# Optimization experiments

Measured on AMD Instinct MI355X. Metric: run time of the kernel, lower is better.

The kernel has to match this reference:

```python
import jax, jax.numpy as jnp
import numpy as np

B, N, D, H = 2, 2048, 1024, 16
HD = D // H  # head dim = 64
SCALING = (D / H) ** 0.5  # sqrt(64) = 8
EPS = 1e-5


def setup_inputs() -> dict:
    key = jax.random.key(0)
    k1, k2, k3 = jax.random.split(key, 3)
    return {
        "z": jax.random.normal(k1, (B, N, D), dtype=jnp.float32),
        "ln_scale": jnp.ones((D,), dtype=jnp.float32),
        "ln_bias": jnp.zeros((D,), dtype=jnp.float32),
        "w_qkv": jax.random.normal(k2, (D, 3 * D), dtype=jnp.float32) * (D ** -0.5),
        "w_proj": jax.random.normal(k3, (D, D), dtype=jnp.float32) * (D ** -0.5),
        "b_proj": jnp.zeros((D,), dtype=jnp.float32),
    }


def reference(z, ln_scale, ln_bias, w_qkv, w_proj, b_proj):
    b, n, d = z.shape
    # LayerNorm (pre-norm)
    mu = jnp.mean(z, axis=-1, keepdims=True)
    var = jnp.mean(jnp.square(z - mu), axis=-1, keepdims=True)
    zn = (z - mu) / jnp.sqrt(var + EPS) * ln_scale + ln_bias
    # QKV projection: [b, n, 3D]
    qkv = zn @ w_qkv
    # einops 'b n (h d qkv_n) -> qkv_n b h n d': qkv index is innermost
    qkv5 = qkv.reshape(b, n, H, HD, 3)  # [b, n, h, d, 3]
    q = jnp.transpose(qkv5[..., 0], (0, 2, 1, 3))  # [b, h, n, d]
    k = jnp.transpose(qkv5[..., 1], (0, 2, 1, 3))
    v = jnp.transpose(qkv5[..., 2], (0, 2, 1, 3))
    # Attention: scores scaled AFTER the matmul, as in the source
    scores = jnp.einsum('bhqd,bhkd->bhqk', q, k) / SCALING
    att = jax.nn.softmax(scores, axis=-1)
    out = jnp.einsum('bhal,bhlv->bhav', att, v)  # [b, h, n, d]
    out = jnp.transpose(out, (0, 2, 1, 3)).reshape(b, n, d)  # merge heads
    out = out @ w_proj + b_proj  # projection (dropout p=0)
    return z + out
```

## Files before the change

kernel.cpp:

```cpp
#include <hip/hip_runtime.h>
#include <stdint.h>
#include <math.h>

typedef unsigned short u16;
typedef float f32x4 __attribute__((ext_vector_type(4)));
typedef __bf16 bf16x8 __attribute__((ext_vector_type(8)));

__device__ __forceinline__ u16 f2bf(float f) {
    union { float f; uint32_t u; } c; c.f = f;
    return (u16)((c.u + 0x7FFFu + ((c.u >> 16) & 1u)) >> 16);
}

__device__ __forceinline__ void gload_lds16(const void* g, void* l) {
    __builtin_amdgcn_global_load_lds(
        (const __attribute__((address_space(1))) unsigned int*)g,
        (__attribute__((address_space(3))) unsigned int*)l, 16, 0, 0);
}

__global__ __launch_bounds__(256) void ln_kernel(const float* __restrict__ z,
                                                 const float* __restrict__ sc,
                                                 const float* __restrict__ bs,
                                                 u16* __restrict__ zn) {
    const int row = blockIdx.x, tid = threadIdx.x;
    const float4 v = ((const float4*)(z + row * 1024))[tid];
    float s = v.x + v.y + v.z + v.w;
    #pragma unroll
    for (int off = 32; off > 0; off >>= 1) s += __shfl_xor(s, off);
    __shared__ float red[8];
    if ((tid & 63) == 0) red[tid >> 6] = s;
    __syncthreads();
    const float mean = (red[0] + red[1] + red[2] + red[3]) * (1.0f / 1024.0f);
    const float dx = v.x - mean, dy = v.y - mean, dz = v.z - mean, dw = v.w - mean;
    float q = dx * dx + dy * dy + dz * dz + dw * dw;
    #pragma unroll
    for (int off = 32; off > 0; off >>= 1) q += __shfl_xor(q, off);
    if ((tid & 63) == 0) red[4 + (tid >> 6)] = q;
    __syncthreads();
    const float var = (red[4] + red[5] + red[6] + red[7]) * (1.0f / 1024.0f);
    const float rstd = rsqrtf(var + 1e-5f);
    const float4 scv = ((const float4*)sc)[tid];
    const float4 bsv = ((const float4*)bs)[tid];
    const u16 o0 = f2bf(dx * rstd * scv.x + bsv.x);
    const u16 o1 = f2bf(dy * rstd * scv.y + bsv.y);
    const u16 o2 = f2bf(dz * rstd * scv.z + bsv.z);
    const u16 o3 = f2bf(dw * rstd * scv.w + bsv.w);
    uint2 pk;
    pk.x = (uint32_t)o0 | ((uint32_t)o1 << 16);
    pk.y = (uint32_t)o2 | ((uint32_t)o3 << 16);
    *(uint2*)&zn[row * 1024 + tid * 4] = pk;
}

__global__ __launch_bounds__(256) void transpose_cast(const float* __restrict__ in,
                                                      u16* __restrict__ out,
                                                      int K, int N, int permute) {
    __shared__ float t[32][33];
    const int tid = threadIdx.x;
    const int j = tid & 31, i0 = tid >> 5;
    const int kb = blockIdx.y * 32, nb = blockIdx.x * 32;
    #pragma unroll
    for (int p = 0; p < 4; ++p) {
        int r = i0 + p * 8;
        t[r][j] = in[(size_t)(kb + r) * N + nb + j];
    }
    __syncthreads();
    #pragma unroll
    for (int p = 0; p < 4; ++p) {
        int r = i0 + p * 8;
        int c = nb + r;
        int np = c;
        if (permute) {
            int h = c / 192, rem = c - h * 192;
            int d = rem / 3, s = rem - d * 3;
            np = s * 1024 + h * 64 + d;
        }
        out[(size_t)np * K + kb + j] = f2bf(t[j][r]);
    }
}

__global__ __launch_bounds__(256) void gemm_qkv(const u16* __restrict__ A,
                                                const u16* __restrict__ Bt,
                                                u16* __restrict__ qbuf,
                                                u16* __restrict__ kbuf,
                                                u16* __restrict__ vbuf) {
    __shared__ __align__(16) u16 As[128 * 32];
    __shared__ __align__(16) u16 Bs[128 * 32];
    const int tid = threadIdx.x;
    const int wave = tid >> 6, lane = tid & 63;
    const int quad = lane >> 4, l16 = lane & 15;
    const int wm = (wave >> 1) * 64, wn = (wave & 1) * 64;
    const int row0 = blockIdx.x * 128, col0 = blockIdx.y * 128;
    const int gr = lane >> 2, gc = (lane & 3) * 8;
    f32x4 acc[4][4] = {};
    for (int kt = 0; kt < 1024; kt += 32) {
        __syncthreads();
        #pragma unroll
        for (int i = 0; i < 2; ++i) {
            const int rb = wave * 16 + i * 64;
            gload_lds16(&A[(size_t)(row0 + rb + gr) * 1024 + kt + gc], &As[rb * 32]);
            gload_lds16(&Bt[(size_t)(col0 + rb + gr) * 1024 + kt + gc], &Bs[rb * 32]);
        }
        __syncthreads();
        bf16x8 ax[4], bx[4];
        #pragma unroll
        for (int t = 0; t < 4; ++t) {
            ax[t] = *(const bf16x8*)&As[(wm + t * 16 + l16) * 32 + quad * 8];
            bx[t] = *(const bf16x8*)&Bs[(wn + t * 16 + l16) * 32 + quad * 8];
        }
        #pragma unroll
        for (int mt = 0; mt < 4; ++mt)
            #pragma unroll
            for (int nt = 0; nt < 4; ++nt)
                acc[mt][nt] = __builtin_amdgcn_mfma_f32_16x16x32_bf16(ax[mt], bx[nt], acc[mt][nt], 0, 0, 0);
    }
    const int s = col0 >> 10;
    u16* const dst = (s == 0) ? qbuf : ((s == 1) ? kbuf : vbuf);
    const float scl = (s == 0) ? 0.125f * 1.44269504088896f : 1.0f;
    #pragma unroll
    for (int mt = 0; mt < 4; ++mt) {
        #pragma unroll
        for (int nt = 0; nt < 4; ++nt) {
            #pragma unroll
            for (int e = 0; e < 4; ++e) {
                const int row = row0 + wm + mt * 16 + quad * 4 + e;
                const int col = col0 + wn + nt * 16 + l16;
                const int b = row >> 11, n = row & 2047;
                const int h = (col >> 6) & 15, d = col & 63;
                dst[((size_t)(b * 16 + h) * 2048 + n) * 64 + d] = f2bf(acc[mt][nt][e] * scl);
            }
        }
    }
}

__global__ __launch_bounds__(256) void transpose_v(const u16* __restrict__ vbuf,
                                                   u16* __restrict__ vT) {
    __shared__ u16 t[64][72];
    const int tid = threadIdx.x;
    const int bh = blockIdx.y, nb = blockIdx.x * 64;
    const int r = tid >> 3, c = (tid & 7) * 8;
    #pragma unroll
    for (int i = 0; i < 2; ++i)
        *(uint4*)&t[r + i * 32][c] = *(const uint4*)&vbuf[((size_t)bh * 2048 + nb + r + i * 32) * 64 + c];
    __syncthreads();
    #pragma unroll
    for (int i = 0; i < 2; ++i) {
        const int d = r + i * 32;
        u16 tmp[8];
        #pragma unroll
        for (int j = 0; j < 8; ++j) tmp[j] = t[c + j][d];
        *(uint4*)&vT[((size_t)bh * 64 + d) * 2048 + nb + c] = *(uint4*)tmp;
    }
}

__global__ __launch_bounds__(256) void attn_kernel(const u16* __restrict__ qb,
                                                   const u16* __restrict__ kb,
                                                   const u16* __restrict__ vT,
                                                   u16* __restrict__ att_out) {
    __shared__ __align__(16) u16 Ks[128 * 64];
    __shared__ __align__(16) u16 Vs[64 * 128];
    const int tid = threadIdx.x;
    const int wave = tid >> 6, lane = tid & 63;
    const int quad = lane >> 4, l16 = lane & 15;
    const int qt = blockIdx.x, bh = blockIdx.y;
    const int b = bh >> 4, h = bh & 15;

    const u16* qrowA = &qb[(size_t)(bh * 2048 + qt * 128 + wave * 32 + l16) * 64];
    const bf16x8 qA0 = *(const bf16x8*)&qrowA[quad * 8];
    const bf16x8 qA1 = *(const bf16x8*)&qrowA[32 + quad * 8];
    const u16* qrowB = qrowA + 16 * 64;
    const bf16x8 qB0 = *(const bf16x8*)&qrowB[quad * 8];
    const bf16x8 qB1 = *(const bf16x8*)&qrowB[32 + quad * 8];

    const u16* ksrc[4];
    const u16* vsrc[4];
    #pragma unroll
    for (int j = 0; j < 4; ++j) {
        const int p = 8 * wave + 32 * j + (lane >> 3);
        const int kr = (p & 0x60) | ((p & 12) << 1) | ((p & 16) >> 2) | (p & 3);
        const int gk = (lane & 7) ^ (p & 7);
        ksrc[j] = kb + ((size_t)bh * 2048 + kr) * 64 + gk * 8;
        const int d = 4 * wave + 16 * j + (lane >> 4);
        const int gv = (lane & 15) ^ (d & 15);
        vsrc[j] = vT + ((size_t)bh * 64 + d) * 2048 + gv * 8;
    }

    f32x4 oA[4] = {}, oB[4] = {};
    f32x4 lA = {}, lB = {};
    bf16x8 ones;
    #pragma unroll
    for (int i = 0; i < 8; ++i) ones[i] = (__bf16)1.0f;

    for (int kt = 0; kt < 16; ++kt) {
        __syncthreads();
        #pragma unroll
        for (int j = 0; j < 4; ++j) {
            gload_lds16(ksrc[j], &Ks[(8 * wave + 32 * j) * 64]);
            gload_lds16(vsrc[j], &Vs[(4 * wave + 16 * j) * 128]);
            ksrc[j] += 128 * 64;
            vsrc[j] += 128;
        }
        __syncthreads();

        f32x4 sA[8] = {}, sB[8] = {};
        #pragma unroll
        for (int nt = 0; nt < 8; ++nt) {
            const int r = nt * 16 + l16;
            const bf16x8 k0 = *(const bf16x8*)&Ks[r * 64 + (((quad) ^ (r & 7)) << 3)];
            const bf16x8 k1 = *(const bf16x8*)&Ks[r * 64 + (((quad + 4) ^ (r & 7)) << 3)];
            sA[nt] = __builtin_amdgcn_mfma_f32_16x16x32_bf16(k0, qA0, sA[nt], 0, 0, 0);
            sA[nt] = __builtin_amdgcn_mfma_f32_16x16x32_bf16(k1, qA1, sA[nt], 0, 0, 0);
            sB[nt] = __builtin_amdgcn_mfma_f32_16x16x32_bf16(k0, qB0, sB[nt], 0, 0, 0);
            sB[nt] = __builtin_amdgcn_mfma_f32_16x16x32_bf16(k1, qB1, sB[nt], 0, 0, 0);
        }

        bf16x8 apA[4], apB[4];
        #pragma unroll
        for (int nt = 0; nt < 8; ++nt) {
            #pragma unroll
            for (int e = 0; e < 4; ++e) {
                apA[nt >> 1][(nt & 1) * 4 + e] = (__bf16)exp2f(sA[nt][e]);
                apB[nt >> 1][(nt & 1) * 4 + e] = (__bf16)exp2f(sB[nt][e]);
            }
        }

        #pragma unroll
        for (int vt = 0; vt < 4; ++vt) {
            const int dd = vt * 16 + l16;
            #pragma unroll
            for (int c = 0; c < 4; ++c) {
                const bf16x8 vf = *(const bf16x8*)&Vs[dd * 128 + (((c * 4 + quad) ^ l16) << 3)];
                oA[vt] = __builtin_amdgcn_mfma_f32_16x16x32_bf16(apA[c], vf, oA[vt], 0, 0, 0);
                oB[vt] = __builtin_amdgcn_mfma_f32_16x16x32_bf16(apB[c], vf, oB[vt], 0, 0, 0);
            }
        }
        #pragma unroll
        for (int c = 0; c < 4; ++c) {
            lA = __builtin_amdgcn_mfma_f32_16x16x32_bf16(apA[c], ones, lA, 0, 0, 0);
            lB = __builtin_amdgcn_mfma_f32_16x16x32_bf16(apB[c], ones, lB, 0, 0, 0);
        }
    }

    #pragma unroll
    for (int e = 0; e < 4; ++e) {
        const float invA = 1.0f / lA[e];
        const float invB = 1.0f / lB[e];
        const int nA = qt * 128 + wave * 32 + quad * 4 + e;
        #pragma unroll
        for (int vt = 0; vt < 4; ++vt) {
            att_out[(size_t)(b * 2048 + nA) * 1024 + h * 64 + vt * 16 + l16] = f2bf(oA[vt][e] * invA);
            att_out[(size_t)(b * 2048 + nA + 16) * 1024 + h * 64 + vt * 16 + l16] = f2bf(oB[vt][e] * invB);
        }
    }
}

__global__ __launch_bounds__(256) void gemm_proj(const u16* __restrict__ A,
                                                 const u16* __restrict__ Bt,
                                                 const float* __restrict__ bias,
                                                 const float* __restrict__ z,
                                                 float* __restrict__ out) {
    __shared__ __align__(16) u16 As[64 * 32];
    __shared__ __align__(16) u16 Bs[128 * 32];
    const int tid = threadIdx.x;
    const int wave = tid >> 6, lane = tid & 63;
    const int quad = lane >> 4, l16 = lane & 15;
    const int wm = (wave >> 1) * 32, wn = (wave & 1) * 64;
    const int row0 = blockIdx.x * 64, col0 = blockIdx.y * 128;
    const int gr = lane >> 2, gc = (lane & 3) * 8;
    f32x4 acc[2][4] = {};
    for (int kt = 0; kt < 1024; kt += 32) {
        __syncthreads();
        gload_lds16(&A[(size_t)(row0 + wave * 16 + gr) * 1024 + kt + gc], &As[(wave * 16) * 32]);
        #pragma unroll
        for (int i = 0; i < 2; ++i) {
            const int rb = wave * 16 + i * 64;
            gload_lds16(&Bt[(size_t)(col0 + rb + gr) * 1024 + kt + gc], &Bs[rb * 32]);
        }
        __syncthreads();
        bf16x8 ax[2], bx[4];
        #pragma unroll
        for (int t = 0; t < 2; ++t)
            ax[t] = *(const bf16x8*)&As[(wm + t * 16 + l16) * 32 + quad * 8];
        #pragma unroll
        for (int t = 0; t < 4; ++t)
            bx[t] = *(const bf16x8*)&Bs[(wn + t * 16 + l16) * 32 + quad * 8];
        #pragma unroll
        for (int mt = 0; mt < 2; ++mt)
            #pragma unroll
            for (int nt = 0; nt < 4; ++nt)
                acc[mt][nt] = __builtin_amdgcn_mfma_f32_16x16x32_bf16(ax[mt], bx[nt], acc[mt][nt], 0, 0, 0);
    }
    #pragma unroll
    for (int mt = 0; mt < 2; ++mt) {
        #pragma unroll
        for (int nt = 0; nt < 4; ++nt) {
            #pragma unroll
            for (int e = 0; e < 4; ++e) {
                const int row = row0 + wm + mt * 16 + quad * 4 + e;
                const int col = col0 + wn + nt * 16 + l16;
                out[(size_t)row * 1024 + col] = acc[mt][nt][e] + bias[col] + z[(size_t)row * 1024 + col];
            }
        }
    }
}

extern "C" void kernel_launch(void* const* d_in, const int* in_sizes, int n_in,
                              void* d_out, int out_size, void* d_ws, size_t ws_size,
                              hipStream_t stream) {
    const float* z        = (const float*)d_in[0];
    const float* ln_scale = (const float*)d_in[1];
    const float* ln_bias  = (const float*)d_in[2];
    const float* w_qkv    = (const float*)d_in[3];
    const float* w_proj   = (const float*)d_in[4];
    const float* b_proj   = (const float*)d_in[5];
    float* out = (float*)d_out;

    char* ws = (char*)d_ws;
    u16* zn     = (u16*)(ws);
    u16* vT     = (u16*)(ws);
    u16* wqkvT  = (u16*)(ws + (8u << 20));
    u16* wprojT = (u16*)(ws + (14u << 20));
    u16* qbuf   = (u16*)(ws + (16u << 20));
    u16* kbuf   = (u16*)(ws + (24u << 20));
    u16* vbuf   = (u16*)(ws + (32u << 20));
    u16* att_o  = (u16*)(ws + (40u << 20));

    ln_kernel<<<dim3(4096), 256, 0, stream>>>(z, ln_scale, ln_bias, zn);
    transpose_cast<<<dim3(96, 32), 256, 0, stream>>>(w_qkv, wqkvT, 1024, 3072, 1);
    transpose_cast<<<dim3(32, 32), 256, 0, stream>>>(w_proj, wprojT, 1024, 1024, 0);
    gemm_qkv<<<dim3(32, 24), 256, 0, stream>>>(zn, wqkvT, qbuf, kbuf, vbuf);
    transpose_v<<<dim3(32, 32), 256, 0, stream>>>(vbuf, vT);
    attn_kernel<<<dim3(16, 32), 256, 0, stream>>>(qbuf, kbuf, vT, att_o);
    gemm_proj<<<dim3(64, 8), 256, 0, stream>>>(att_o, wprojT, b_proj, z, out);
}
```

Baseline: 209.7 us.

## Restructure attention into split-KV two-wave blocks with double-buffered LDS prefetch

The attention kernel moves from 256-thread blocks covering 128 queries to 128-thread blocks covering 64 queries. Each of the two waves handles half of every 128-key tile for all 64 queries, and the partial outputs and row sums are combined through LDS at the end. K/V tiles are double-buffered in LDS so the next tile is prefetched while the current one is computed, which drops one barrier per iteration. The grid doubles to 1024 blocks. In exchange it uses 64KB of LDS per block, limits occupancy with launch_bounds(128,1), and adds a final cross-wave reduction.

```diff
diff --git a/kernel.cpp b/kernel.cpp
--- a/kernel.cpp
+++ b/kernel.cpp
@@ -151,103 +151,147 @@
     }
 }
 
-__global__ __launch_bounds__(256) void attn_kernel(const u16* __restrict__ qb,
-                                                   const u16* __restrict__ kb,
-                                                   const u16* __restrict__ vT,
-                                                   u16* __restrict__ att_out) {
-    __shared__ __align__(16) u16 Ks[128 * 64];
-    __shared__ __align__(16) u16 Vs[64 * 128];
-    const int tid = threadIdx.x;
-    const int wave = tid >> 6, lane = tid & 63;
+__global__ __launch_bounds__(128, 1) void attn_kernel(const u16* __restrict__ qb,
+                                                      const u16* __restrict__ kb,
+                                                      const u16* __restrict__ vT,
+                                                      u16* __restrict__ att_out) {
+    __shared__ __align__(16) u16 smem[32768];
+    const int tid = threadIdx.x;
+    const int w = tid >> 6, lane = tid & 63;
     const int quad = lane >> 4, l16 = lane & 15;
     const int qt = blockIdx.x, bh = blockIdx.y;
     const int b = bh >> 4, h = bh & 15;
 
-    const u16* qrowA = &qb[(size_t)(bh * 2048 + qt * 128 + wave * 32 + l16) * 64];
-    const bf16x8 qA0 = *(const bf16x8*)&qrowA[quad * 8];
-    const bf16x8 qA1 = *(const bf16x8*)&qrowA[32 + quad * 8];
-    const u16* qrowB = qrowA + 16 * 64;
-    const bf16x8 qB0 = *(const bf16x8*)&qrowB[quad * 8];
-    const bf16x8 qB1 = *(const bf16x8*)&qrowB[32 + quad * 8];
-
-    const u16* ksrc[4];
-    const u16* vsrc[4];
-    #pragma unroll
-    for (int j = 0; j < 4; ++j) {
-        const int p = 8 * wave + 32 * j + (lane >> 3);
-        const int kr = (p & 0x60) | ((p & 12) << 1) | ((p & 16) >> 2) | (p & 3);
-        const int gk = (lane & 7) ^ (p & 7);
-        ksrc[j] = kb + ((size_t)bh * 2048 + kr) * 64 + gk * 8;
-        const int d = 4 * wave + 16 * j + (lane >> 4);
-        const int gv = (lane & 15) ^ (d & 15);
-        vsrc[j] = vT + ((size_t)bh * 64 + d) * 2048 + gv * 8;
-    }
-
-    f32x4 oA[4] = {}, oB[4] = {};
-    f32x4 lA = {}, lB = {};
+    bf16x8 qf[4][2];
+    #pragma unroll
+    for (int g = 0; g < 4; ++g) {
+        const u16* qr = qb + ((size_t)bh * 2048 + qt * 64 + g * 16 + l16) * 64;
+        qf[g][0] = *(const bf16x8*)&qr[quad * 8];
+        qf[g][1] = *(const bf16x8*)&qr[32 + quad * 8];
+    }
+
+    const int p0 = 8 * w + (lane >> 3);
+    const int gk = (lane & 7) ^ ((lane >> 3) & 7);
+    const int lanepart_k = ((p0 & 12) << 1) + (p0 & 3);
+    const size_t kbh = (size_t)bh * 2048 * 64;
+    const int dl = 4 * w + (lane >> 4);
+    const int gv0 = (lane & 15) ^ dl;
+    const int gv1 = (lane & 15) ^ (8 + dl);
+    const size_t vbh = (size_t)bh * 64 * 2048;
+    const int jk[8] = {0, 4, 32, 36, 64, 68, 96, 100};
+
+    f32x4 o[4][4] = {};
+    f32x4 lacc[4] = {};
     bf16x8 ones;
     #pragma unroll
     for (int i = 0; i < 8; ++i) ones[i] = (__bf16)1.0f;
 
+    {
+        u16* KsB = smem;
+        u16* VsB = smem + 16384;
+        #pragma unroll
+        for (int j = 0; j < 8; ++j)
+            gload_lds16(kb + kbh + (size_t)((jk[j] + lanepart_k) * 64 + gk * 8),
+                        KsB + (j * 16 + 8 * w) * 64);
+        #pragma unroll
+        for (int j = 0; j < 8; ++j)
+            gload_lds16(vT + vbh + (size_t)((j * 8 + dl) * 2048 + ((j & 1) ? gv1 : gv0) * 8),
+                        VsB + (j * 8 + 4 * w) * 128);
+    }
+
     for (int kt = 0; kt < 16; ++kt) {
         __syncthreads();
-        #pragma unroll
-        for (int j = 0; j < 4; ++j) {
-            gload_lds16(ksrc[j], &Ks[(8 * wave + 32 * j) * 64]);
-            gload_lds16(vsrc[j], &Vs[(4 * wave + 16 * j) * 128]);
-            ksrc[j] += 128 * 64;
-            vsrc[j] += 128;
-        }
-        __syncthreads();
-
-        f32x4 sA[8] = {}, sB[8] = {};
-        #pragma unroll
-        for (int nt = 0; nt < 8; ++nt) {
-            const int r = nt * 16 + l16;
-            const bf16x8 k0 = *(const bf16x8*)&Ks[r * 64 + (((quad) ^ (r & 7)) << 3)];
-            const bf16x8 k1 = *(const bf16x8*)&Ks[r * 64 + (((quad + 4) ^ (r & 7)) << 3)];
-            sA[nt] = __builtin_amdgcn_mfma_f32_16x16x32_bf16(k0, qA0, sA[nt], 0, 0, 0);
-            sA[nt] = __builtin_amdgcn_mfma_f32_16x16x32_bf16(k1, qA1, sA[nt], 0, 0, 0);
-            sB[nt] = __builtin_amdgcn_mfma_f32_16x16x32_bf16(k0, qB0, sB[nt], 0, 0, 0);
-            sB[nt] = __builtin_amdgcn_mfma_f32_16x16x32_bf16(k1, qB1, sB[nt], 0, 0, 0);
-        }
-
-        bf16x8 apA[4], apB[4];
-        #pragma unroll
-        for (int nt = 0; nt < 8; ++nt) {
-            #pragma unroll
-            for (int e = 0; e < 4; ++e) {
-                apA[nt >> 1][(nt & 1) * 4 + e] = (__bf16)exp2f(sA[nt][e]);
-                apB[nt >> 1][(nt & 1) * 4 + e] = (__bf16)exp2f(sB[nt][e]);
-            }
+        if (kt < 15) {
+            const int nb_ = (kt + 1) & 1;
+            u16* KsB = smem + nb_ * 8192;
+            u16* VsB = smem + 16384 + nb_ * 8192;
+            const int ko = (kt + 1) * 128;
+            #pragma unroll
+            for (int j = 0; j < 8; ++j)
+                gload_lds16(kb + kbh + (size_t)((ko + jk[j] + lanepart_k) * 64 + gk * 8),
+                            KsB + (j * 16 + 8 * w) * 64);
+            #pragma unroll
+            for (int j = 0; j < 8; ++j)
+                gload_lds16(vT + vbh + (size_t)((j * 8 + dl) * 2048 + ko + ((j & 1) ? gv1 : gv0) * 8),
+                            VsB + (j * 8 + 4 * w) * 128);
+        }
+        const u16* KsB = smem + (kt & 1) * 8192;
+        const u16* VsB = smem + 16384 + (kt & 1) * 8192;
+
+        bf16x8 kf[4][2];
+        #pragma unroll
+        for (int nt = 0; nt < 4; ++nt) {
+            const int r = (4 * w + nt) * 16 + l16;
+            kf[nt][0] = *(const bf16x8*)&KsB[r * 64 + ((quad ^ (r & 7)) << 3)];
+            kf[nt][1] = *(const bf16x8*)&KsB[r * 64 + (((quad + 4) ^ (r & 7)) << 3)];
+        }
+
+        bf16x8 ap[4][2];
+        #pragma unroll
+        for (int g = 0; g < 4; ++g) {
+            f32x4 s[4] = {};
+            #pragma unroll
+            for (int nt = 0; nt < 4; ++nt) {
+                s[nt] = __builtin_amdgcn_mfma_f32_16x16x32_bf16(kf[nt][0], qf[g][0], s[nt], 0, 0, 0);
+                s[nt] = __builtin_amdgcn_mfma_f32_16x16x32_bf16(kf[nt][1], qf[g][1], s[nt], 0, 0, 0);
+            }
+            #pragma unroll
+            for (int nt = 0; nt < 4; ++nt)
+                #pragma unroll
+                for (int e = 0; e < 4; ++e)
+                    ap[g][nt >> 1][(nt & 1) * 4 + e] = (__bf16)exp2f(s[nt][e]);
         }
 
         #pragma unroll
         for (int vt = 0; vt < 4; ++vt) {
-            const int dd = vt * 16 + l16;
-            #pragma unroll
-            for (int c = 0; c < 4; ++c) {
-                const bf16x8 vf = *(const bf16x8*)&Vs[dd * 128 + (((c * 4 + quad) ^ l16) << 3)];
-                oA[vt] = __builtin_amdgcn_mfma_f32_16x16x32_bf16(apA[c], vf, oA[vt], 0, 0, 0);
-                oB[vt] = __builtin_amdgcn_mfma_f32_16x16x32_bf16(apB[c], vf, oB[vt], 0, 0, 0);
-            }
-        }
-        #pragma unroll
-        for (int c = 0; c < 4; ++c) {
-            lA = __builtin_amdgcn_mfma_f32_16x16x32_bf16(apA[c], ones, lA, 0, 0, 0);
-            lB = __builtin_amdgcn_mfma_f32_16x16x32_bf16(apB[c], ones, lB, 0, 0, 0);
-        }
-    }
-
-    #pragma unroll
-    for (int e = 0; e < 4; ++e) {
-        const float invA = 1.0f / lA[e];
-        const float invB = 1.0f / lB[e];
-        const int nA = qt * 128 + wave * 32 + quad * 4 + e;
-        #pragma unroll
-        for (int vt = 0; vt < 4; ++vt) {
-            att_out[(size_t)(b * 2048 + nA) * 1024 + h * 64 + vt * 16 + l16] = f2bf(oA[vt][e] * invA);
-            att_out[(size_t)(b * 2048 + nA + 16) * 1024 + h * 64 + vt * 16 + l16] = f2bf(oB[vt][e] * invB);
+            const int d = vt * 16 + l16;
+            #pragma unroll
+            for (int cl = 0; cl < 2; ++cl) {
+                const bf16x8 vf = *(const bf16x8*)&VsB[d * 128 + ((((2 * w + cl) * 4 + quad) ^ l16) << 3)];
+                #pragma unroll
+                for (int g = 0; g < 4; ++g)
+                    o[g][vt] = __builtin_amdgcn_mfma_f32_16x16x32_bf16(ap[g][cl], vf, o[g][vt], 0, 0, 0);
+            }
+        }
+        #pragma unroll
+        for (int cl = 0; cl < 2; ++cl)
+            #pragma unroll
+            for (int g = 0; g < 4; ++g)
+                lacc[g] = __builtin_amdgcn_mfma_f32_16x16x32_bf16(ap[g][cl], ones, lacc[g], 0, 0, 0);
+    }
+
+    __syncthreads();
+    float* Ox = (float*)smem;
+    float* lx = Ox + 4 * 16 * 68;
+    const int give0 = (w == 0) ? 2 : 0;
+    #pragma unroll
+    for (int gi = 0; gi < 2; ++gi) {
+        const int g = give0 + gi;
+        #pragma unroll
+        for (int vt = 0; vt < 4; ++vt)
+            #pragma unroll
+            for (int e = 0; e < 4; ++e)
+                Ox[(g * 16 + quad * 4 + e) * 68 + vt * 16 + l16] = o[g][vt][e];
+        if (l16 == 0) {
+            #pragma unroll
+            for (int e = 0; e < 4; ++e) lx[g * 16 + quad * 4 + e] = lacc[g][e];
+        }
+    }
+    __syncthreads();
+    const int keep0 = (w == 0) ? 0 : 2;
+    #pragma unroll
+    for (int gi = 0; gi < 2; ++gi) {
+        const int g = keep0 + gi;
+        #pragma unroll
+        for (int e = 0; e < 4; ++e) {
+            const float lt = lacc[g][e] + lx[g * 16 + quad * 4 + e];
+            const float inv = 1.0f / lt;
+            const int n = qt * 64 + g * 16 + quad * 4 + e;
+            #pragma unroll
+            for (int vt = 0; vt < 4; ++vt) {
+                const float ov = o[g][vt][e] + Ox[(g * 16 + quad * 4 + e) * 68 + vt * 16 + l16];
+                att_out[(size_t)(b * 2048 + n) * 1024 + h * 64 + vt * 16 + l16] = f2bf(ov * inv);
+            }
         }
     }
 }
@@ -328,6 +372,6 @@
     transpose_cast<<<dim3(32, 32), 256, 0, stream>>>(w_proj, wprojT, 1024, 1024, 0);
     gemm_qkv<<<dim3(32, 24), 256, 0, stream>>>(zn, wqkvT, qbuf, kbuf, vbuf);
     transpose_v<<<dim3(32, 32), 256, 0, stream>>>(vbuf, vT);
-    attn_kernel<<<dim3(16, 32), 256, 0, stream>>>(qbuf, kbuf, vT, att_o);
+    attn_kernel<<<dim3(32, 32), 128, 0, stream>>>(qbuf, kbuf, vT, att_o);
     gemm_proj<<<dim3(64, 8), 256, 0, stream>>>(att_o, wprojT, b_proj, z, out);
 }
```

Result: slower. 324.3 us (+54.7%).
